# Kernel optimization log

Measured on AMD Instinct MI355X. Metric: run time of the kernel, lower is better.

## Reference

```python
import jax, jax.numpy as jnp
import numpy as np

V, E, H, L, T_MAX = 50257, 384, 6, 6, 256
HS = E // H  # 64
LN_EPS = 1e-5


def _ln(x, g, b):
    mu = jnp.mean(x, axis=-1, keepdims=True)
    var = jnp.mean(jnp.square(x - mu), axis=-1, keepdims=True)
    return (x - mu) * jax.lax.rsqrt(var + LN_EPS) * g + b


def setup_inputs() -> dict:
    key = jax.random.key(0)
    ks = jax.random.split(key, 24)
    B, T = 16, 256
    s_emb = 1.0 / np.sqrt(E)
    inp = {
        'idx': jax.random.randint(ks[0], (B, T), 0, V),
        'targets': jax.random.randint(ks[1], (B, T), 0, V),
        'tok_emb': jax.random.normal(ks[2], (V, E), jnp.float32) * 0.02,
        'pos_emb': jax.random.normal(ks[3], (V, E), jnp.float32) * 0.02,
        'Wq': jax.random.normal(ks[4], (L, E, E), jnp.float32) * s_emb,
        'Wk': jax.random.normal(ks[5], (L, E, E), jnp.float32) * s_emb,
        'Wv': jax.random.normal(ks[6], (L, E, E), jnp.float32) * s_emb,
        'Wproj': jax.random.normal(ks[7], (L, E, E), jnp.float32) * s_emb,
        'bproj': jnp.zeros((L, E), jnp.float32),
        'W1': jax.random.normal(ks[8], (L, E, 4 * E), jnp.float32) * s_emb,
        'b1': jnp.zeros((L, 4 * E), jnp.float32),
        'W2': jax.random.normal(ks[9], (L, 4 * E, E), jnp.float32) * (0.5 * s_emb),
        'b2': jnp.zeros((L, E), jnp.float32),
        'ln1_g': jnp.ones((L, E), jnp.float32), 'ln1_b': jnp.zeros((L, E), jnp.float32),
        'ln2_g': jnp.ones((L, E), jnp.float32), 'ln2_b': jnp.zeros((L, E), jnp.float32),
        'lnf_g': jnp.ones((E,), jnp.float32), 'lnf_b': jnp.zeros((E,), jnp.float32),
        'Whead': jax.random.normal(ks[10], (E, V), jnp.float32) * s_emb,
        'bhead': jnp.zeros((V,), jnp.float32),
    }
    return inp


def _forward(idx, targets, tok_emb, pos_emb, Wq, Wk, Wv, Wproj, bproj,
             W1, b1, W2, b2, ln1_g, ln1_b, ln2_g, ln2_b, lnf_g, lnf_b, Whead, bhead):
    B, T = idx.shape
    x = tok_emb[idx] + pos_emb[:T]                      # [B,T,E]
    causal = jnp.tril(jnp.ones((T, T), bool))           # tril mask
    scale = E ** (-0.5)                                 # NOTE: scaled by n_embd, as in source
    for l in range(L):
        h = _ln(x, ln1_g[l], ln1_b[l])
        q = (h @ Wq[l]).reshape(B, T, H, HS)
        k = (h @ Wk[l]).reshape(B, T, H, HS)
        v = (h @ Wv[l]).reshape(B, T, H, HS)
        wei = jnp.einsum('bqhd,bkhd->bhqk', q, k) * scale
        wei = jnp.where(causal, wei, -jnp.inf)
        wei = jax.nn.softmax(wei, axis=-1)              # dropout: eval mode (identity)
        att = jnp.einsum('bhqk,bkhd->bqhd', wei, v).reshape(B, T, E)
        x = x + att @ Wproj[l] + bproj[l]
        h2 = _ln(x, ln2_g[l], ln2_b[l])
        x = x + jax.nn.relu(h2 @ W1[l] + b1[l]) @ W2[l] + b2[l]
    x = _ln(x, lnf_g, lnf_b)
    logits = x @ Whead + bhead                          # [B,T,V]
    logp = jax.nn.log_softmax(logits, axis=-1)
    loss = -jnp.mean(jnp.take_along_axis(logp, targets[..., None], axis=-1))
    return logits, loss


def reference(idx, targets, tok_emb, pos_emb, Wq, Wk, Wv, Wproj, bproj,
              W1, b1, W2, b2, ln1_g, ln1_b, ln2_g, ln2_b, lnf_g, lnf_b, Whead, bhead):
    return _forward(idx, targets, tok_emb, pos_emb, Wq, Wk, Wv, Wproj, bproj,
                    W1, b1, W2, b2, ln1_g, ln1_b, ln2_g, ln2_b, lnf_g, lnf_b, Whead, bhead)
```

## Files before the change

### kernel.cpp

```cpp
#include <hip/hip_runtime.h>

#define NL 6
#define EMB 384
#define NH 6
#define HSZ 64
#define TT 256
#define NTOK 4096
#define VOC 50257
#define VOCP 50304
#define FF 1536
#define QKVW 1152
#define NCH 393

typedef __attribute__((ext_vector_type(8))) short bf16x8;
typedef __attribute__((ext_vector_type(4))) float f32x4;

__device__ __forceinline__ short f2bf(float f) {
  unsigned u = __float_as_uint(f);
  u = (u + 0x7fffu + ((u >> 16) & 1u)) >> 16;
  return (short)u;
}

__device__ __forceinline__ int swz16(int b) {
  return b ^ (((((b >> 6) ^ (b >> 8)) & 1) << 4) | (((b >> 7) & 1) << 5));
}

__device__ __forceinline__ void gl16(const void* g, void* l) {
  __builtin_amdgcn_global_load_lds(
      (const __attribute__((address_space(1))) unsigned*)g,
      (__attribute__((address_space(3))) unsigned*)l, 16, 0, 0);
}

__global__ void embed_k(const int* __restrict__ idx, const float* __restrict__ tok,
                        const float* __restrict__ pos, float* __restrict__ x) {
  int row = blockIdx.x, col = threadIdx.x;
  int t = idx[row];
  x[(size_t)row * EMB + col] = tok[(size_t)t * EMB + col] + pos[(size_t)(row & 255) * EMB + col];
}

__global__ __launch_bounds__(256) void tcast_k(const float* __restrict__ src, short* __restrict__ dst,
                                               int K, int N, long sstr, long dstr) {
  src += (size_t)blockIdx.z * sstr;
  dst += (size_t)blockIdx.z * dstr;
  __shared__ float tile[32][33];
  int lx = threadIdx.x & 31, ly = threadIdx.x >> 5;
  int k0 = blockIdx.y << 5, n0 = blockIdx.x << 5;
#pragma unroll
  for (int j = 0; j < 4; ++j) {
    int k = k0 + ly + (j << 3), n = n0 + lx;
    tile[ly + (j << 3)][lx] = (n < N) ? src[(size_t)k * N + n] : 0.f;
  }
  __syncthreads();
#pragma unroll
  for (int j = 0; j < 4; ++j) {
    int n = n0 + ly + (j << 3), k = k0 + lx;
    dst[(size_t)n * K + k] = f2bf(tile[lx][ly + (j << 3)]);
  }
}

__global__ __launch_bounds__(256) void ln_k(const float* __restrict__ x, const float* __restrict__ g,
                                            const float* __restrict__ b, short* __restrict__ out) {
  int wave = threadIdx.x >> 6, lane = threadIdx.x & 63;
  int row = (blockIdx.x << 2) + wave;
  const float* p = x + (size_t)row * EMB;
  float v[6]; float s = 0.f;
#pragma unroll
  for (int j = 0; j < 6; ++j) { v[j] = p[lane + (j << 6)]; s += v[j]; }
#pragma unroll
  for (int o = 32; o; o >>= 1) s += __shfl_xor(s, o, 64);
  float mu = s * (1.f / EMB);
  float q = 0.f;
#pragma unroll
  for (int j = 0; j < 6; ++j) { float d = v[j] - mu; q += d * d; }
#pragma unroll
  for (int o = 32; o; o >>= 1) q += __shfl_xor(q, o, 64);
  float rstd = rsqrtf(q * (1.f / EMB) + 1e-5f);
  short* op = out + (size_t)row * EMB;
#pragma unroll
  for (int j = 0; j < 6; ++j) {
    int c = lane + (j << 6);
    op[c] = f2bf((v[j] - mu) * rstd * g[c] + b[c]);
  }
}

__global__ __launch_bounds__(256) void vtrans_k(const short* __restrict__ qkv, short* __restrict__ vt) {
  int bh = blockIdx.y; int b = bh / NH, h = bh % NH;
  int t0 = blockIdx.x << 6;
  __shared__ short tile[64][72];
  int tid = threadIdx.x;
#pragma unroll
  for (int pass = 0; pass < 2; ++pass) {
    int tl = pass * 32 + (tid >> 3);
    int d0 = (tid & 7) << 3;
    uint4 v = *(const uint4*)&qkv[((size_t)(b * TT + t0 + tl)) * QKVW + 2 * EMB + h * HSZ + d0];
    *(uint4*)&tile[tl][d0] = v;
  }
  __syncthreads();
  int d = tid >> 2, tc = (tid & 3) << 4;
  short* dst = &vt[((size_t)bh * 64 + d) * TT + t0 + tc];
#pragma unroll
  for (int j = 0; j < 16; ++j) dst[j] = tile[tc + j][d];
}

__global__ __launch_bounds__(256) void attn_k(const short* __restrict__ qkv,
                                              const short* __restrict__ vt,
                                              short* __restrict__ att) {
  const float SCALE = 0.051031036307982884f;
  int qt = blockIdx.x, bh = blockIdx.y;
  int b = bh / NH, h = bh % NH;
  __shared__ short P[64][260];
  int tid = threadIdx.x, w = tid >> 6, lane = tid & 63;
  int lr = lane & 15, g = lane >> 4;
  int qbase = qt * 64 + w * 16;

  const short* qrow = qkv + (size_t)(b * TT + qbase + lr) * QKVW + h * HSZ;
  bf16x8 qa0 = *(const bf16x8*)(qrow + g * 8);
  bf16x8 qa1 = *(const bf16x8*)(qrow + 32 + g * 8);

  f32x4 zero = {0.f, 0.f, 0.f, 0.f};
  f32x4 s[16];
#pragma unroll
  for (int kf = 0; kf < 16; ++kf) s[kf] = zero;
#pragma unroll
  for (int kf = 0; kf < 16; ++kf) {
    const short* krow = qkv + (size_t)(b * TT + kf * 16 + lr) * QKVW + EMB + h * HSZ;
    bf16x8 kb0 = *(const bf16x8*)(krow + g * 8);
    bf16x8 kb1 = *(const bf16x8*)(krow + 32 + g * 8);
    s[kf] = __builtin_amdgcn_mfma_f32_16x16x32_bf16(qa0, kb0, s[kf], 0, 0, 0);
    s[kf] = __builtin_amdgcn_mfma_f32_16x16x32_bf16(qa1, kb1, s[kf], 0, 0, 0);
  }

#pragma unroll
  for (int i = 0; i < 4; ++i) {
    int qg = qbase + g * 4 + i;
    float m = -1e30f;
#pragma unroll
    for (int kf = 0; kf < 16; ++kf) {
      float v = s[kf][i] * SCALE;
      if (kf * 16 + lr > qg) v = -1e30f;
      s[kf][i] = v;
      m = fmaxf(m, v);
    }
#pragma unroll
    for (int o = 8; o; o >>= 1) m = fmaxf(m, __shfl_xor(m, o, 64));
    float sum = 0.f;
#pragma unroll
    for (int kf = 0; kf < 16; ++kf) {
      float e = __expf(s[kf][i] - m);
      s[kf][i] = e;
      sum += e;
    }
#pragma unroll
    for (int o = 8; o; o >>= 1) sum += __shfl_xor(sum, o, 64);
    float inv = 1.f / sum;
#pragma unroll
    for (int kf = 0; kf < 16; ++kf)
      P[w * 16 + g * 4 + i][kf * 16 + lr] = f2bf(s[kf][i] * inv);
  }

  f32x4 o4[4];
#pragma unroll
  for (int nf = 0; nf < 4; ++nf) o4[nf] = zero;
  const short* vbase = vt + (size_t)bh * 64 * TT;
#pragma unroll
  for (int ks = 0; ks < 8; ++ks) {
    bf16x8 pa = *(const bf16x8*)&P[w * 16 + lr][ks * 32 + g * 8];
#pragma unroll
    for (int nf = 0; nf < 4; ++nf) {
      bf16x8 vb = *(const bf16x8*)(vbase + (size_t)(nf * 16 + lr) * TT + ks * 32 + g * 8);
      o4[nf] = __builtin_amdgcn_mfma_f32_16x16x32_bf16(pa, vb, o4[nf], 0, 0, 0);
    }
  }
#pragma unroll
  for (int nf = 0; nf < 4; ++nf)
#pragma unroll
    for (int i = 0; i < 4; ++i)
      att[(size_t)(b * TT + qbase + g * 4 + i) * EMB + h * HSZ + nf * 16 + lr] = f2bf(o4[nf][i]);
}

#define GM_QKV 0
#define GM_RESID 3
#define GM_FC1 4
#define GM_HEAD 5

template <int MODE>
__global__ __launch_bounds__(256) void gemm_k(
    const short* __restrict__ Ag, const short* __restrict__ Btg, void* Cg,
    const float* __restrict__ bias, const float* resid,
    int K, int lda, int ldb, int ldc, float scale,
    float* __restrict__ pm, float* __restrict__ ps) {
  __shared__ alignas(1024) char smem[2 * 2 * 128 * 32 * 2];
  short* sA = (short*)smem;
  short* sB = (short*)(smem + 16384);
  int tid = threadIdx.x;
  int bm = blockIdx.x, bn = blockIdx.y;
  int wave = tid >> 6, lane = tid & 63;
  int wm = wave >> 1, wn = wave & 1;
  int lr = lane & 15, kq = lane >> 4;
  size_t lda2 = (size_t)lda * 2, ldb2 = (size_t)ldb * 2;

  int p = wave * 1024 + lane * 16;
  int q = swz16(p);
  int srow = q >> 6, scb = q & 63;
  const char* gA = (const char*)Ag + (size_t)(bm * 128 + srow) * lda2 + scb;
  const char* gB = (const char*)Btg + (size_t)(bn * 128 + srow) * ldb2 + scb;
  char* lA0 = (char*)sA + wave * 1024; char* lA1 = lA0 + 4096;
  char* lB0 = (char*)sB + wave * 1024; char* lB1 = lB0 + 4096;

  const char* apf[4]; const char* bpf[4];
#pragma unroll
  for (int f = 0; f < 4; ++f) {
    int La = (wm * 64 + f * 16 + lr) * 64 + kq * 16;
    apf[f] = (const char*)sA + swz16(La);
    int Lb = (wn * 64 + f * 16 + lr) * 64 + kq * 16;
    bpf[f] = (const char*)sB + swz16(Lb);
  }

  f32x4 zero = {0.f, 0.f, 0.f, 0.f};
  f32x4 acc[4][4];
#pragma unroll
  for (int i = 0; i < 4; ++i)
#pragma unroll
    for (int j = 0; j < 4; ++j) acc[i][j] = zero;

  gl16(gA, lA0); gl16(gA + 64 * lda2, lA1);
  gl16(gB, lB0); gl16(gB + 64 * ldb2, lB1);
  __syncthreads();

  int nt = K >> 5;
  for (int t = 0; t < nt; ++t) {
    int cur = (t & 1) << 13, nxt = (~t & 1) << 13;
    if (t + 1 < nt) {
      const char* ga2 = gA + (size_t)(t + 1) * 64;
      const char* gb2 = gB + (size_t)(t + 1) * 64;
      gl16(ga2, lA0 + nxt); gl16(ga2 + 64 * lda2, lA1 + nxt);
      gl16(gb2, lB0 + nxt); gl16(gb2 + 64 * ldb2, lB1 + nxt);
    }
    bf16x8 af[4], bfr[4];
#pragma unroll
    for (int f = 0; f < 4; ++f) {
      af[f] = *(const bf16x8*)(apf[f] + cur);
      bfr[f] = *(const bf16x8*)(bpf[f] + cur);
    }
#pragma unroll
    for (int i = 0; i < 4; ++i)
#pragma unroll
      for (int j = 0; j < 4; ++j)
        acc[i][j] = __builtin_amdgcn_mfma_f32_16x16x32_bf16(af[i], bfr[j], acc[i][j], 0, 0, 0);
    __syncthreads();
  }

  int row0 = bm * 128 + wm * 64 + (kq << 2);
  int col0 = bn * 128 + wn * 64 + lr;

  if constexpr (MODE == GM_QKV) {
    short* C = (short*)Cg;
#pragma unroll
    for (int fm = 0; fm < 4; ++fm)
#pragma unroll
      for (int fn = 0; fn < 4; ++fn) {
        int c = col0 + fn * 16;
#pragma unroll
        for (int i = 0; i < 4; ++i)
          C[(size_t)(row0 + fm * 16 + i) * ldc + c] = f2bf(acc[fm][fn][i]);
      }
  } else if constexpr (MODE == GM_FC1) {
    short* C = (short*)Cg;
#pragma unroll
    for (int fm = 0; fm < 4; ++fm)
#pragma unroll
      for (int fn = 0; fn < 4; ++fn) {
        int c = col0 + fn * 16;
        float bv = bias[c];
#pragma unroll
        for (int i = 0; i < 4; ++i)
          C[(size_t)(row0 + fm * 16 + i) * ldc + c] = f2bf(fmaxf(acc[fm][fn][i] + bv, 0.f));
      }
  } else if constexpr (MODE == GM_RESID) {
    float* C = (float*)Cg;
#pragma unroll
    for (int fm = 0; fm < 4; ++fm)
#pragma unroll
      for (int fn = 0; fn < 4; ++fn) {
        int c = col0 + fn * 16;
        float bv = bias[c];
#pragma unroll
        for (int i = 0; i < 4; ++i) {
          size_t o = (size_t)(row0 + fm * 16 + i) * ldc + c;
          C[o] = resid[o] + acc[fm][fn][i] + bv;
        }
      }
  } else if constexpr (MODE == GM_HEAD) {
    __shared__ float redm[2][2][64];
    __shared__ float reds[2][2][64];
    float* C = (float*)Cg;
    bool okv[4]; float bv[4];
#pragma unroll
    for (int fn = 0; fn < 4; ++fn) {
      int c = col0 + fn * 16;
      okv[fn] = c < VOC;
      bv[fn] = okv[fn] ? bias[c] : 0.f;
    }
#pragma unroll
    for (int fm = 0; fm < 4; ++fm)
#pragma unroll
      for (int fn = 0; fn < 4; ++fn)
#pragma unroll
        for (int i = 0; i < 4; ++i) acc[fm][fn][i] += bv[fn];
#pragma unroll
    for (int fm = 0; fm < 4; ++fm)
#pragma unroll
      for (int i = 0; i < 4; ++i) {
        float v0 = okv[0] ? acc[fm][0][i] : -1e30f;
        float v1 = okv[1] ? acc[fm][1][i] : -1e30f;
        float v2 = okv[2] ? acc[fm][2][i] : -1e30f;
        float v3 = okv[3] ? acc[fm][3][i] : -1e30f;
        float mx = fmaxf(fmaxf(v0, v1), fmaxf(v2, v3));
#pragma unroll
        for (int o = 8; o; o >>= 1) mx = fmaxf(mx, __shfl_xor(mx, o, 64));
        float sm = __expf(v0 - mx) + __expf(v1 - mx) + __expf(v2 - mx) + __expf(v3 - mx);
#pragma unroll
        for (int o = 8; o; o >>= 1) sm += __shfl_xor(sm, o, 64);
        if (lr == 0) {
          int rl = fm * 16 + (kq << 2) + i;
          redm[wm][wn][rl] = mx; reds[wm][wn][rl] = sm;
        }
      }
    __syncthreads();
    if (tid < 128) {
      int wmm = tid >> 6, rl = tid & 63;
      float m0 = redm[wmm][0][rl], m1 = redm[wmm][1][rl];
      float s0 = reds[wmm][0][rl], s1 = reds[wmm][1][rl];
      float M = fmaxf(m0, m1);
      float S = s0 * __expf(m0 - M) + s1 * __expf(m1 - M);
      int r = bm * 128 + wmm * 64 + rl;
      pm[(size_t)r * NCH + bn] = M;
      ps[(size_t)r * NCH + bn] = S;
    }
    float (*cst)[132] = reinterpret_cast<float(*)[132]>(smem);
    int colbase = bn * 128;
#pragma unroll
    for (int c = 0; c < 4; ++c) {
      __syncthreads();
      if (wm == (c >> 1)) {
        int fmb = (c & 1) * 2;
#pragma unroll
        for (int f2 = 0; f2 < 2; ++f2)
#pragma unroll
          for (int fn = 0; fn < 4; ++fn)
#pragma unroll
            for (int i = 0; i < 4; ++i)
              cst[f2 * 16 + kq * 4 + i][wn * 64 + fn * 16 + lr] = acc[fmb + f2][fn][i];
      }
      __syncthreads();
      int rowg = bm * 128 + c * 32;
#pragma unroll
      for (int pp = 0; pp < 16; ++pp) {
        int idx = pp * 256 + tid;
        int rw = idx >> 7, cc = idx & 127;
        int gc = colbase + cc;
        if (gc < VOC)
          __builtin_nontemporal_store(cst[rw][cc], &C[(size_t)(rowg + rw) * VOC + gc]);
      }
    }
  }
}

__global__ __launch_bounds__(256) void lsecomb_k(const float* __restrict__ pm, const float* __restrict__ ps,
                                                 const float* __restrict__ logits, const int* __restrict__ tgt,
                                                 float* __restrict__ rowloss) {
  int wave = threadIdx.x >> 6, lane = threadIdx.x & 63;
  int r = (blockIdx.x << 2) + wave;
  float m = -1e30f, s = 0.f;
  for (int i = lane; i < NCH; i += 64) {
    float bm = pm[(size_t)r * NCH + i], bs = ps[(size_t)r * NCH + i];
    float M = fmaxf(m, bm);
    s = s * __expf(m - M) + bs * __expf(bm - M);
    m = M;
  }
#pragma unroll
  for (int o = 32; o; o >>= 1) {
    float mo = __shfl_xor(m, o, 64), so = __shfl_xor(s, o, 64);
    float M = fmaxf(m, mo);
    s = s * __expf(m - M) + so * __expf(mo - M);
    m = M;
  }
  if (lane == 0) rowloss[r] = m + __logf(s) - logits[(size_t)r * VOC + tgt[r]];
}

__global__ __launch_bounds__(256) void loss_final_k(const float* __restrict__ rowloss,
                                                    float* __restrict__ out) {
  __shared__ float sb[256];
  int tid = threadIdx.x;
  float s = 0.f;
  for (int i = tid; i < NTOK; i += 256) s += rowloss[i];
  sb[tid] = s;
  __syncthreads();
  for (int o = 128; o; o >>= 1) {
    if (tid < o) sb[tid] += sb[tid + o];
    __syncthreads();
  }
  if (tid == 0) out[0] = sb[0] * (1.f / NTOK);
}

extern "C" void kernel_launch(void* const* d_in, const int* in_sizes, int n_in,
                              void* d_out, int out_size, void* d_ws, size_t ws_size,
                              hipStream_t stream) {
  const int* idx = (const int*)d_in[0];
  const int* tgt = (const int*)d_in[1];
  const float* tok = (const float*)d_in[2];
  const float* pos = (const float*)d_in[3];
  const float* Wq = (const float*)d_in[4];
  const float* Wk = (const float*)d_in[5];
  const float* Wv = (const float*)d_in[6];
  const float* Wp = (const float*)d_in[7];
  const float* bp = (const float*)d_in[8];
  const float* W1 = (const float*)d_in[9];
  const float* b1 = (const float*)d_in[10];
  const float* W2 = (const float*)d_in[11];
  const float* b2 = (const float*)d_in[12];
  const float* ln1g = (const float*)d_in[13];
  const float* ln1b = (const float*)d_in[14];
  const float* ln2g = (const float*)d_in[15];
  const float* ln2b = (const float*)d_in[16];
  const float* lnfg = (const float*)d_in[17];
  const float* lnfb = (const float*)d_in[18];
  const float* Wh = (const float*)d_in[19];
  const float* bh = (const float*)d_in[20];

  char* wp = (char*)d_ws;
  auto take = [&](size_t elems, size_t esz) {
    void* r = (void*)wp;
    wp += (elems * esz + 255) & ~(size_t)255;
    return r;
  };
  short* wqkv_t = (short*)take((size_t)NL * QKVW * EMB, 2);
  short* wproj_t = (short*)take((size_t)NL * EMB * EMB, 2);
  short* w1_t = (short*)take((size_t)NL * FF * EMB, 2);
  short* w2_t = (short*)take((size_t)NL * EMB * FF, 2);
  short* whead_t = (short*)take((size_t)VOCP * EMB, 2);
  float* x = (float*)take((size_t)NTOK * EMB, 4);
  short* hb = (short*)take((size_t)NTOK * EMB, 2);
  short* qkv = (short*)take((size_t)NTOK * QKVW, 2);
  float* sc = (float*)take((size_t)96 * TT * TT, 4);
  short* vt = (short*)take((size_t)96 * 64 * TT, 2);
  short* att = (short*)take((size_t)NTOK * EMB, 2);
  short* f1 = (short*)take((size_t)NTOK * FF, 2);
  float* rl = (float*)take((size_t)NTOK, 4);

  float* pm = sc;
  float* ps = sc + (size_t)NTOK * NCH;

  tcast_k<<<dim3(12, 12, NL), 256, 0, stream>>>(Wq, wqkv_t, EMB, EMB, (long)EMB * EMB, (long)QKVW * EMB);
  tcast_k<<<dim3(12, 12, NL), 256, 0, stream>>>(Wk, wqkv_t + EMB * EMB, EMB, EMB, (long)EMB * EMB, (long)QKVW * EMB);
  tcast_k<<<dim3(12, 12, NL), 256, 0, stream>>>(Wv, wqkv_t + 2 * EMB * EMB, EMB, EMB, (long)EMB * EMB, (long)QKVW * EMB);
  tcast_k<<<dim3(12, 12, NL), 256, 0, stream>>>(Wp, wproj_t, EMB, EMB, (long)EMB * EMB, (long)EMB * EMB);
  tcast_k<<<dim3(48, 12, NL), 256, 0, stream>>>(W1, w1_t, EMB, FF, (long)EMB * FF, (long)FF * EMB);
  tcast_k<<<dim3(12, 48, NL), 256, 0, stream>>>(W2, w2_t, FF, EMB, (long)FF * EMB, (long)EMB * FF);
  tcast_k<<<dim3(VOCP / 32, 12, 1), 256, 0, stream>>>(Wh, whead_t, EMB, VOC, 0, 0);

  embed_k<<<NTOK, EMB, 0, stream>>>(idx, tok, pos, x);

  for (int l = 0; l < NL; ++l) {
    ln_k<<<NTOK / 4, 256, 0, stream>>>(x, ln1g + l * EMB, ln1b + l * EMB, hb);
    gemm_k<GM_QKV><<<dim3(32, 9), 256, 0, stream>>>(hb, wqkv_t + (size_t)l * QKVW * EMB, qkv,
        nullptr, nullptr, EMB, EMB, EMB, QKVW, 0.f, nullptr, nullptr);
    vtrans_k<<<dim3(4, 96), 256, 0, stream>>>(qkv, vt);
    attn_k<<<dim3(4, 96), 256, 0, stream>>>(qkv, vt, att);
    gemm_k<GM_RESID><<<dim3(32, 3), 256, 0, stream>>>(att, wproj_t + (size_t)l * EMB * EMB, x,
        bp + l * EMB, x, EMB, EMB, EMB, EMB, 0.f, nullptr, nullptr);
    ln_k<<<NTOK / 4, 256, 0, stream>>>(x, ln2g + l * EMB, ln2b + l * EMB, hb);
    gemm_k<GM_FC1><<<dim3(32, 12), 256, 0, stream>>>(hb, w1_t + (size_t)l * FF * EMB, f1,
        b1 + l * FF, nullptr, EMB, EMB, EMB, FF, 0.f, nullptr, nullptr);
    gemm_k<GM_RESID><<<dim3(32, 3), 256, 0, stream>>>(f1, w2_t + (size_t)l * EMB * FF, x,
        b2 + l * EMB, x, FF, FF, FF, EMB, 0.f, nullptr, nullptr);
  }

  ln_k<<<NTOK / 4, 256, 0, stream>>>(x, lnfg, lnfb, hb);
  gemm_k<GM_HEAD><<<dim3(32, NCH), 256, 0, stream>>>(hb, whead_t, (float*)d_out,
      bh, nullptr, EMB, EMB, EMB, VOC, 0.f, pm, ps);
  lsecomb_k<<<NTOK / 4, 256, 0, stream>>>(pm, ps, (const float*)d_out, tgt, rl);
  loss_final_k<<<1, 256, 0, stream>>>(rl, (float*)d_out + (size_t)NTOK * VOC);
}
```

Measured before the change: 1.171 ms.

## Skip masked key tiles in attention and use 64x64 tiles for residual GEMMs

Attention is templated on the number of key fragments, so each query tile only computes QK^T and PV over the causally visible keys rather than all 256. The projection and FC2 residual GEMMs move from a 128x128 tile kernel with a 96-block grid to a new 64x64 double-buffered kernel with 384 blocks, to fill more compute units on the MI355X. The trade-offs are more code variants and less per-block data reuse in the smaller-tile GEMM.

```diff
diff --git a/kernel.cpp b/kernel.cpp
--- a/kernel.cpp
+++ b/kernel.cpp
@@ -102,14 +102,14 @@
   for (int j = 0; j < 16; ++j) dst[j] = tile[tc + j][d];
 }
 
-__global__ __launch_bounds__(256) void attn_k(const short* __restrict__ qkv,
-                                              const short* __restrict__ vt,
-                                              short* __restrict__ att) {
+template <int KFB>
+__device__ __forceinline__ void attn_body(const short* __restrict__ qkv,
+                                          const short* __restrict__ vt,
+                                          short* __restrict__ att,
+                                          short (*P)[260], int qt, int bh, int tid) {
   const float SCALE = 0.051031036307982884f;
-  int qt = blockIdx.x, bh = blockIdx.y;
   int b = bh / NH, h = bh % NH;
-  __shared__ short P[64][260];
-  int tid = threadIdx.x, w = tid >> 6, lane = tid & 63;
+  int w = tid >> 6, lane = tid & 63;
   int lr = lane & 15, g = lane >> 4;
   int qbase = qt * 64 + w * 16;
 
@@ -118,11 +118,11 @@
   bf16x8 qa1 = *(const bf16x8*)(qrow + 32 + g * 8);
 
   f32x4 zero = {0.f, 0.f, 0.f, 0.f};
-  f32x4 s[16];
-#pragma unroll
-  for (int kf = 0; kf < 16; ++kf) s[kf] = zero;
-#pragma unroll
-  for (int kf = 0; kf < 16; ++kf) {
+  f32x4 s[KFB];
+#pragma unroll
+  for (int kf = 0; kf < KFB; ++kf) s[kf] = zero;
+#pragma unroll
+  for (int kf = 0; kf < KFB; ++kf) {
     const short* krow = qkv + (size_t)(b * TT + kf * 16 + lr) * QKVW + EMB + h * HSZ;
     bf16x8 kb0 = *(const bf16x8*)(krow + g * 8);
     bf16x8 kb1 = *(const bf16x8*)(krow + 32 + g * 8);
@@ -135,7 +135,7 @@
     int qg = qbase + g * 4 + i;
     float m = -1e30f;
 #pragma unroll
-    for (int kf = 0; kf < 16; ++kf) {
+    for (int kf = 0; kf < KFB; ++kf) {
       float v = s[kf][i] * SCALE;
       if (kf * 16 + lr > qg) v = -1e30f;
       s[kf][i] = v;
@@ -145,7 +145,7 @@
     for (int o = 8; o; o >>= 1) m = fmaxf(m, __shfl_xor(m, o, 64));
     float sum = 0.f;
 #pragma unroll
-    for (int kf = 0; kf < 16; ++kf) {
+    for (int kf = 0; kf < KFB; ++kf) {
       float e = __expf(s[kf][i] - m);
       s[kf][i] = e;
       sum += e;
@@ -154,7 +154,7 @@
     for (int o = 8; o; o >>= 1) sum += __shfl_xor(sum, o, 64);
     float inv = 1.f / sum;
 #pragma unroll
-    for (int kf = 0; kf < 16; ++kf)
+    for (int kf = 0; kf < KFB; ++kf)
       P[w * 16 + g * 4 + i][kf * 16 + lr] = f2bf(s[kf][i] * inv);
   }
 
@@ -163,7 +163,7 @@
   for (int nf = 0; nf < 4; ++nf) o4[nf] = zero;
   const short* vbase = vt + (size_t)bh * 64 * TT;
 #pragma unroll
-  for (int ks = 0; ks < 8; ++ks) {
+  for (int ks = 0; ks < KFB / 2; ++ks) {
     bf16x8 pa = *(const bf16x8*)&P[w * 16 + lr][ks * 32 + g * 8];
 #pragma unroll
     for (int nf = 0; nf < 4; ++nf) {
@@ -178,8 +178,18 @@
       att[(size_t)(b * TT + qbase + g * 4 + i) * EMB + h * HSZ + nf * 16 + lr] = f2bf(o4[nf][i]);
 }
 
+__global__ __launch_bounds__(256) void attn_k(const short* __restrict__ qkv,
+                                              const short* __restrict__ vt,
+                                              short* __restrict__ att) {
+  __shared__ short P[64][260];
+  int qt = blockIdx.x, bh = blockIdx.y, tid = threadIdx.x;
+  if (qt == 0)      attn_body<4>(qkv, vt, att, P, 0, bh, tid);
+  else if (qt == 1) attn_body<8>(qkv, vt, att, P, 1, bh, tid);
+  else if (qt == 2) attn_body<12>(qkv, vt, att, P, 2, bh, tid);
+  else              attn_body<16>(qkv, vt, att, P, 3, bh, tid);
+}
+
 #define GM_QKV 0
-#define GM_RESID 3
 #define GM_FC1 4
 #define GM_HEAD 5
 
@@ -275,20 +285,6 @@
 #pragma unroll
         for (int i = 0; i < 4; ++i)
           C[(size_t)(row0 + fm * 16 + i) * ldc + c] = f2bf(fmaxf(acc[fm][fn][i] + bv, 0.f));
-      }
-  } else if constexpr (MODE == GM_RESID) {
-    float* C = (float*)Cg;
-#pragma unroll
-    for (int fm = 0; fm < 4; ++fm)
-#pragma unroll
-      for (int fn = 0; fn < 4; ++fn) {
-        int c = col0 + fn * 16;
-        float bv = bias[c];
-#pragma unroll
-        for (int i = 0; i < 4; ++i) {
-          size_t o = (size_t)(row0 + fm * 16 + i) * ldc + c;
-          C[o] = resid[o] + acc[fm][fn][i] + bv;
-        }
       }
   } else if constexpr (MODE == GM_HEAD) {
     __shared__ float redm[2][2][64];
@@ -364,6 +360,82 @@
       }
     }
   }
+}
+
+__global__ __launch_bounds__(256) void gemm64_k(
+    const short* __restrict__ Ag, const short* __restrict__ Btg, float* __restrict__ C,
+    const float* __restrict__ bias, const float* __restrict__ resid,
+    int K, int lda, int ldb, int ldc) {
+  __shared__ alignas(1024) short sA[2 * 64 * 32];
+  __shared__ alignas(1024) short sB[2 * 64 * 32];
+  int tid = threadIdx.x;
+  int bm = blockIdx.x, bn = blockIdx.y;
+  int wave = tid >> 6, lane = tid & 63;
+  int wm = wave >> 1, wn = wave & 1;
+  int lr = lane & 15, kq = lane >> 4;
+  size_t lda2 = (size_t)lda * 2, ldb2 = (size_t)ldb * 2;
+
+  int p = wave * 1024 + lane * 16;
+  int q = swz16(p);
+  int srow = q >> 6, scb = q & 63;
+  const char* gA = (const char*)Ag + (size_t)(bm * 64 + srow) * lda2 + scb;
+  const char* gB = (const char*)Btg + (size_t)(bn * 64 + srow) * ldb2 + scb;
+  char* lA0 = (char*)sA + wave * 1024;
+  char* lB0 = (char*)sB + wave * 1024;
+
+  const char* apf[2]; const char* bpf[2];
+#pragma unroll
+  for (int f = 0; f < 2; ++f) {
+    apf[f] = (const char*)sA + swz16((wm * 32 + f * 16 + lr) * 64 + kq * 16);
+    bpf[f] = (const char*)sB + swz16((wn * 32 + f * 16 + lr) * 64 + kq * 16);
+  }
+
+  f32x4 zero = {0.f, 0.f, 0.f, 0.f};
+  f32x4 acc[2][2];
+#pragma unroll
+  for (int i = 0; i < 2; ++i)
+#pragma unroll
+    for (int j = 0; j < 2; ++j) acc[i][j] = zero;
+
+  gl16(gA, lA0);
+  gl16(gB, lB0);
+  __syncthreads();
+
+  int nt = K >> 5;
+  for (int t = 0; t < nt; ++t) {
+    int cur = (t & 1) << 12, nxt = (~t & 1) << 12;
+    if (t + 1 < nt) {
+      gl16(gA + (size_t)(t + 1) * 64, lA0 + nxt);
+      gl16(gB + (size_t)(t + 1) * 64, lB0 + nxt);
+    }
+    bf16x8 af[2], bfr[2];
+#pragma unroll
+    for (int f = 0; f < 2; ++f) {
+      af[f] = *(const bf16x8*)(apf[f] + cur);
+      bfr[f] = *(const bf16x8*)(bpf[f] + cur);
+    }
+#pragma unroll
+    for (int i = 0; i < 2; ++i)
+#pragma unroll
+      for (int j = 0; j < 2; ++j)
+        acc[i][j] = __builtin_amdgcn_mfma_f32_16x16x32_bf16(af[i], bfr[j], acc[i][j], 0, 0, 0);
+    __syncthreads();
+  }
+
+  int row0 = bm * 64 + wm * 32 + (kq << 2);
+  int col0 = bn * 64 + wn * 32 + lr;
+#pragma unroll
+  for (int fm = 0; fm < 2; ++fm)
+#pragma unroll
+    for (int fn = 0; fn < 2; ++fn) {
+      int c = col0 + fn * 16;
+      float bv = bias[c];
+#pragma unroll
+      for (int i = 0; i < 4; ++i) {
+        size_t o = (size_t)(row0 + fm * 16 + i) * ldc + c;
+        C[o] = resid[o] + acc[fm][fn][i] + bv;
+      }
+    }
 }
 
 __global__ __launch_bounds__(256) void lsecomb_k(const float* __restrict__ pm, const float* __restrict__ ps,
@@ -467,13 +539,13 @@
         nullptr, nullptr, EMB, EMB, EMB, QKVW, 0.f, nullptr, nullptr);
     vtrans_k<<<dim3(4, 96), 256, 0, stream>>>(qkv, vt);
     attn_k<<<dim3(4, 96), 256, 0, stream>>>(qkv, vt, att);
-    gemm_k<GM_RESID><<<dim3(32, 3), 256, 0, stream>>>(att, wproj_t + (size_t)l * EMB * EMB, x,
-        bp + l * EMB, x, EMB, EMB, EMB, EMB, 0.f, nullptr, nullptr);
+    gemm64_k<<<dim3(64, 6), 256, 0, stream>>>(att, wproj_t + (size_t)l * EMB * EMB, x,
+        bp + l * EMB, x, EMB, EMB, EMB, EMB);
     ln_k<<<NTOK / 4, 256, 0, stream>>>(x, ln2g + l * EMB, ln2b + l * EMB, hb);
     gemm_k<GM_FC1><<<dim3(32, 12), 256, 0, stream>>>(hb, w1_t + (size_t)l * FF * EMB, f1,
         b1 + l * FF, nullptr, EMB, EMB, EMB, FF, 0.f, nullptr, nullptr);
-    gemm_k<GM_RESID><<<dim3(32, 3), 256, 0, stream>>>(f1, w2_t + (size_t)l * EMB * FF, x,
-        b2 + l * EMB, x, FF, FF, FF, EMB, 0.f, nullptr, nullptr);
+    gemm64_k<<<dim3(64, 6), 256, 0, stream>>>(f1, w2_t + (size_t)l * EMB * FF, x,
+        b2 + l * EMB, x, FF, FF, FF, EMB);
   }
 
   ln_k<<<NTOK / 4, 256, 0, stream>>>(x, lnfg, lnfb, hb);
```

Result: faster. 970.8 us, median of 2 (-17.1%).
